# Optimization experiments

Measured on AMD Instinct MI355X. Metric: run time of the kernel, lower is better.

## Reference

```python
import jax, jax.numpy as jnp
import numpy as np

N = 200_000      # nodes
E = 6_400_000    # edges (avg degree 32)
G = 2_000        # graphs
SD = 10          # state_dim
ROUNDS = 3


def setup_inputs() -> dict:
    key = jax.random.key(0)
    ks = jax.random.split(key, 10)
    node_coordinates = jax.random.normal(ks[0], (N, 3), dtype=jnp.float32)
    node_graph_index = jnp.sort(jax.random.randint(ks[1], (N,), 0, G))
    node_from = jax.random.randint(ks[2], (E,), 0, N)
    node_to = jax.random.randint(ks[3], (E,), 0, N)
    edge_lengths = jax.random.uniform(ks[4], (E, 1), dtype=jnp.float32)
    edge_vectors = jax.random.normal(ks[5], (E, 3), dtype=jnp.float32)
    # message net: Linear(14 -> 10), torch default uniform init
    lim = 1.0 / np.sqrt(SD + 4)
    W_msg = jax.random.uniform(ks[6], (SD + 4, SD), minval=-lim, maxval=lim, dtype=jnp.float32)
    b_msg = jax.random.uniform(ks[7], (SD,), minval=-lim, maxval=lim, dtype=jnp.float32)
    # output net: Linear(10 -> 4), xavier_normal weight, default bias
    W_out = jax.random.normal(ks[8], (SD, 4), dtype=jnp.float32) * np.float32(np.sqrt(2.0 / (SD + 4)))
    lim_o = 1.0 / np.sqrt(SD)
    b_out = jax.random.uniform(ks[9], (4,), minval=-lim_o, maxval=lim_o, dtype=jnp.float32)
    return dict(node_coordinates=node_coordinates, edge_lengths=edge_lengths,
                edge_vectors=edge_vectors, W_msg=W_msg, b_msg=b_msg,
                W_out=W_out, b_out=b_out, node_from=node_from, node_to=node_to,
                node_graph_index=node_graph_index, num_nodes=N, num_graphs=G)


def reference(node_coordinates, edge_lengths, edge_vectors, W_msg, b_msg,
              W_out, b_out, node_from, node_to, node_graph_index,
              num_nodes, num_graphs):
    c_from = node_coordinates[node_from]                      # (E,3) gather
    c_to = node_coordinates[node_to]                          # (E,3) gather
    coord_sum = jnp.sum(jnp.abs(c_from), axis=1, keepdims=True)       # (E,1)
    dot1 = jnp.sum(c_from * c_to, axis=1, keepdims=True)              # (E,1)
    dot2 = jnp.sum(c_from * edge_vectors, axis=1, keepdims=True)      # (E,1)
    geo = jnp.concatenate([edge_lengths, coord_sum, dot1, dot2], axis=1)  # (E,4), identical every round

    state = jnp.zeros((num_nodes, SD), dtype=node_coordinates.dtype)
    for _ in range(ROUNDS):
        inp = jnp.concatenate([state[node_from], geo], axis=1)        # (E,14)
        msg = jnp.tanh(inp @ W_msg + b_msg)                           # (E,10)
        state = state + jax.ops.segment_sum(msg, node_to, num_segments=num_nodes)

    graph_state = jax.ops.segment_sum(state, node_graph_index, num_segments=num_graphs)  # (G,10)
    ev = graph_state @ W_out + b_out                                  # (G,4)
    gamma, v, alpha, beta = jnp.split(ev, 4, axis=1)
    sp = jax.nn.softplus
    return jnp.concatenate([gamma, sp(v), sp(alpha) + 1.0, sp(beta)], axis=1)
```

## Files before the change

kernel.cpp:

```cpp
#include <hip/hip_runtime.h>
#include <hip/hip_fp16.h>
#include <math.h>

#define SD 10
#define BSZ 64
#define EB 512
#define CTHR 1024
#define BINB 9
#define NBIN_MAX 512
#define HSZ 256
#define SCAP 10880

typedef unsigned uvec4 __attribute__((ext_vector_type(4)));
struct rec12 { unsigned x, y, z; };
union U32H2 { unsigned u; __half2 h; };

__device__ __forceinline__ float tanh_fast(float x) {
    float e = __expf(2.0f * x);
    float r = __builtin_amdgcn_rcpf(1.0f + e);
    return 1.0f - 2.0f * r;
}

__device__ __forceinline__ float softplus_f(float x) {
    return fmaxf(x, 0.0f) + log1pf(expf(-fabsf(x)));
}


__global__ __launch_bounds__(256) void coords4_kernel(
    const float* __restrict__ coords, float4* __restrict__ coords4, int N)
{
    int n = blockIdx.x * blockDim.x + threadIdx.x;
    if (n >= N) return;
    float4 c;
    c.x = coords[n * 3 + 0];
    c.y = coords[n * 3 + 1];
    c.z = coords[n * 3 + 2];
    c.w = fabsf(c.x) + fabsf(c.y) + fabsf(c.z);
    coords4[n] = c;
}


__global__ __launch_bounds__(CTHR) void pass1_kernel(
    const float* __restrict__ elen,
    const float* __restrict__ evec,
    const int* __restrict__ nfrom,
    const int* __restrict__ nto,
    unsigned* __restrict__ s1addr,
    rec12* __restrict__ payA,
    int E, int NBIN)
{
    __shared__ unsigned hbin[NBIN_MAX];
    __shared__ unsigned curbin[NBIN_MAX];
    int b = blockIdx.x, t = threadIdx.x;
    long long ebeg = (long long)E * b / EB;
    long long eend = (long long)E * (b + 1) / EB;

    if (t < NBIN_MAX) hbin[t] = 0;
    __syncthreads();
    for (long long e = ebeg + t; e < eend; e += CTHR)
        atomicAdd(&hbin[((unsigned)__builtin_nontemporal_load(&nto[e])) >> BINB], 1u);
    __syncthreads();
    {
        unsigned v = (t < NBIN_MAX) ? hbin[t] : 0u;
        for (int d = 1; d < NBIN_MAX; d <<= 1) {
            unsigned x = (t < NBIN_MAX && t >= d) ? hbin[t - d] : 0u;
            __syncthreads();
            if (t < NBIN_MAX) hbin[t] += x;
            __syncthreads();
        }
        if (t < NBIN_MAX) curbin[t] = (unsigned)ebeg + hbin[t] - v;
    }
    __syncthreads();
    if (t < NBIN) s1addr[(size_t)t * EB + b] = curbin[t];
    if (t == 0)  s1addr[(size_t)NBIN * EB + b] = (unsigned)eend;
    __syncthreads();

    for (long long e = ebeg + t; e < eend; e += CTHR) {
        int nf = __builtin_nontemporal_load(&nfrom[e]);
        int nt = __builtin_nontemporal_load(&nto[e]);
        float l  = __builtin_nontemporal_load(&elen[e]);
        float ex = __builtin_nontemporal_load(&evec[e * 3 + 0]);
        float ey = __builtin_nontemporal_load(&evec[e * 3 + 1]);
        float ez = __builtin_nontemporal_load(&evec[e * 3 + 2]);
        unsigned bin = ((unsigned)nt) >> BINB;
        unsigned pos = atomicAdd(&curbin[bin], 1u);
        U32H2 a, c;
        a.h = __floats2half2_rn(l, ex);
        c.h = __floats2half2_rn(ey, ez);
        rec12 r;
        r.x = (unsigned)nf | (((unsigned)nt & ((1u << BINB) - 1u)) << 18);
        r.y = a.u;
        r.z = c.u;
        payA[pos] = r;
    }
}

__global__ __launch_bounds__(256) void colsum_kernel(
    const unsigned* __restrict__ s1addr, unsigned* __restrict__ binsum)
{
    __shared__ unsigned red[256];
    int q = blockIdx.x, t = threadIdx.x;
    red[t] = s1addr[(size_t)q * EB + t] + s1addr[(size_t)q * EB + t + 256];
    __syncthreads();
    for (int d = 128; d > 0; d >>= 1) {
        if (t < d) red[t] += red[t + d];
        __syncthreads();
    }
    if (t == 0) binsum[q] = red[0];
}

__global__ __launch_bounds__(256) void binstart_kernel(
    const unsigned* __restrict__ binsum, unsigned* __restrict__ binstart,
    unsigned* __restrict__ nodestart, int NBIN, int E)
{
    int t = threadIdx.x;
    unsigned b0 = binsum[0];
    for (int q = t; q <= NBIN; q += 256) binstart[q] = binsum[q] - b0;
    if (t == 0) nodestart[(size_t)NBIN << BINB] = (unsigned)E;
}

__global__ __launch_bounds__(CTHR) void pass2_kernel(
    const unsigned* __restrict__ s1addr,
    const unsigned* __restrict__ binstart,
    const float4* __restrict__ coords4,
    const rec12* __restrict__ src,
    rec12* __restrict__ dst,
    unsigned* __restrict__ nodestart,
    int NBIN)
{
    __shared__ unsigned segst[EB];
    __shared__ unsigned spref[EB + 1];
    __shared__ unsigned hist[1 << BINB];
    __shared__ unsigned cur[1 << BINB];
    __shared__ rec12 stage[SCAP];
    int q = blockIdx.x, t = threadIdx.x;
    const unsigned KMASK = (1u << BINB) - 1u;

    if (t < EB) {
        unsigned st = s1addr[(size_t)q * EB + t];
        unsigned en = s1addr[(size_t)(q + 1) * EB + t];
        segst[t] = st;
        spref[t] = en - st;
    }
    if (t < (1 << BINB)) hist[t] = 0;
    __syncthreads();
    {
        unsigned v = (t < EB) ? spref[t] : 0u;
        for (int d = 1; d < EB; d <<= 1) {
            unsigned x = (t < EB && t >= d) ? spref[t - d] : 0u;
            __syncthreads();
            if (t < EB) spref[t] += x;
            __syncthreads();
        }
        unsigned incl = (t < EB) ? spref[t] : 0u;
        __syncthreads();
        if (t < EB) spref[t] = incl - v;
        if (t == EB - 1) spref[EB] = incl;
    }
    __syncthreads();
    unsigned len = spref[EB];
    unsigned obase = binstart[q];
    const unsigned* srcw = (const unsigned*)src;

    for (unsigned i = t; i < len; i += CTHR) {
        unsigned lo = 0, hi = EB;
#pragma unroll
        for (int s = 0; s < 9; s++) {
            unsigned mid = (lo + hi) >> 1;
            if (spref[mid] <= i) lo = mid; else hi = mid;
        }
        unsigned x0 = srcw[(size_t)(segst[lo] + (i - spref[lo])) * 3];
        atomicAdd(&hist[(x0 >> 18) & KMASK], 1u);
    }
    __syncthreads();
    unsigned hv = (t < (1 << BINB)) ? hist[t] : 0u;
    __syncthreads();
    for (int d = 1; d < (1 << BINB); d <<= 1) {
        unsigned x = (t < (1 << BINB) && t >= d) ? hist[t - d] : 0u;
        __syncthreads();
        if (t < (1 << BINB)) hist[t] += x;
        __syncthreads();
    }
    if (t < (1 << BINB)) {
        unsigned excl = hist[t] - hv;
        cur[t] = obase + excl;
        nodestart[((size_t)q << BINB) + t] = obase + excl;
    }
    __syncthreads();

    for (int h = 0; h < (1 << BINB) / HSZ; ++h) {
        unsigned kbeg = (unsigned)h * HSZ, kend = kbeg + HSZ;
        unsigned qs = kbeg ? hist[kbeg - 1] : 0u;
        unsigned qe = hist[kend - 1];
        unsigned qlen = qe - qs;
        unsigned qg = obase + qs;
        if (qlen <= (unsigned)SCAP) {
            for (unsigned i = t; i < len; i += CTHR) {
                unsigned lo = 0, hi = EB;
#pragma unroll
                for (int s = 0; s < 9; s++) {
                    unsigned mid = (lo + hi) >> 1;
                    if (spref[mid] <= i) lo = mid; else hi = mid;
                }
                rec12 p = src[segst[lo] + (i - spref[lo])];
                unsigned key = (p.x >> 18) & KMASK;
                if (key >= kbeg && key < kend) {
                    unsigned pos = atomicAdd(&cur[key], 1u);
                    stage[pos - qg] = p;
                }
            }
            __syncthreads();
            unsigned i = t;
            rec12 p0; float4 cf0;
            if (i < qlen) {
                p0 = stage[i];
                cf0 = coords4[p0.x & 0x3FFFFu];
            }
            while (i < qlen) {
                unsigned i1 = i + CTHR;
                rec12 p1 = p0; float4 cf1 = cf0;
                if (i1 < qlen) {
                    p1 = stage[i1];
                    cf1 = coords4[p1.x & 0x3FFFFu];
                }
                unsigned key = (p0.x >> 18) & KMASK;
                unsigned nf = p0.x & 0x3FFFFu;
                unsigned nt = ((unsigned)q << BINB) | key;
                float4 ct = coords4[nt];
                U32H2 ya, za;
                ya.u = p0.y; za.u = p0.z;
                float g0 = __low2float(ya.h), ev0 = __high2float(ya.h);
                float ev1 = __low2float(za.h), ev2 = __high2float(za.h);
                float g2 = cf0.x * ct.x + cf0.y * ct.y + cf0.z * ct.z;
                float g3 = cf0.x * ev0 + cf0.y * ev1 + cf0.z * ev2;
                U32H2 oy, oz;
                oy.h = __floats2half2_rn(g0, cf0.w);
                oz.h = __floats2half2_rn(g2, g3);
                rec12 r;
                r.x = nf | ((nt & (BSZ - 1u)) << 18);
                r.y = oy.u;
                r.z = oz.u;
                dst[qg + i] = r;
                i = i1; p0 = p1; cf0 = cf1;
            }
            __syncthreads();
        } else {
            for (unsigned i = t; i < len; i += CTHR) {
                unsigned lo = 0, hi = EB;
#pragma unroll
                for (int s = 0; s < 9; s++) {
                    unsigned mid = (lo + hi) >> 1;
                    if (spref[mid] <= i) lo = mid; else hi = mid;
                }
                rec12 p = src[segst[lo] + (i - spref[lo])];
                unsigned key = (p.x >> 18) & KMASK;
                if (key >= kbeg && key < kend) {
                    unsigned pos = atomicAdd(&cur[key], 1u);
                    unsigned nf = p.x & 0x3FFFFu;
                    unsigned nt = ((unsigned)q << BINB) | key;
                    float4 cf = coords4[nf];
                    float4 ct = coords4[nt];
                    U32H2 ya, za;
                    ya.u = p.y; za.u = p.z;
                    float g0 = __low2float(ya.h), ev0 = __high2float(ya.h);
                    float ev1 = __low2float(za.h), ev2 = __high2float(za.h);
                    float g2 = cf.x * ct.x + cf.y * ct.y + cf.z * ct.z;
                    float g3 = cf.x * ev0 + cf.y * ev1 + cf.z * ev2;
                    U32H2 oy, oz;
                    oy.h = __floats2half2_rn(g0, cf.w);
                    oz.h = __floats2half2_rn(g2, g3);
                    rec12 r;
                    r.x = nf | ((nt & (BSZ - 1u)) << 18);
                    r.y = oy.u;
                    r.z = oz.u;
                    dst[pos] = r;
                }
            }
            __syncthreads();
        }
    }
}


__global__ __launch_bounds__(256) void wstate_kernel(
    const float* __restrict__ state, const float* __restrict__ Wm,
    const float* __restrict__ bm, __half* __restrict__ wsth, int N)
{
    int n = blockIdx.x * blockDim.x + threadIdx.x;
    if (n >= N) return;
    const float2* sp = (const float2*)(state + (size_t)n * SD);
    float s[SD];
#pragma unroll
    for (int h = 0; h < 5; h++) { float2 v = sp[h]; s[2*h] = v.x; s[2*h+1] = v.y; }
    float t[SD];
#pragma unroll
    for (int j = 0; j < SD; j++) t[j] = bm[j];
#pragma unroll
    for (int k = 0; k < SD; k++) {
#pragma unroll
        for (int j = 0; j < SD; j++) t[j] += s[k] * Wm[k * SD + j];
    }
    unsigned* dp = (unsigned*)(wsth + (size_t)n * SD);
#pragma unroll
    for (int h = 0; h < 5; h++) {
        U32H2 cv;
        cv.h = __floats2half2_rn(t[2*h], t[2*h+1]);
        dp[h] = cv.u;
    }
}

template <bool FIRST>
__global__ __launch_bounds__(256) void round_run_kernel(
    const unsigned* __restrict__ nodestart,
    const rec12* __restrict__ payload,
    const float* __restrict__ Wm,
    const float* __restrict__ bm,
    const __half* __restrict__ wsth,
    const float* __restrict__ state_prev,
    float* __restrict__ state_next,
    int N, int E)
{
    __shared__ float acc[BSZ * SD];
    int k = blockIdx.x;
    for (int i = threadIdx.x; i < BSZ * SD; i += 256) acc[i] = 0.0f;

    int lane = threadIdx.x & 63;
    int wv = threadIdx.x >> 6;
    int grp0 = lane / 10;
    bool active = grp0 < 6;
    int grp = active ? grp0 : 5;
    int j = active ? (lane - grp0 * 10) : (lane - 60);

    float w0 = Wm[10 * SD + j];
    float w1 = Wm[11 * SD + j];
    float w2 = Wm[12 * SD + j];
    float w3 = Wm[13 * SD + j];
    float bb = bm[j];
    __syncthreads();

    unsigned beg = nodestart[(size_t)k << 6];
    unsigned end = nodestart[(size_t)(k + 1) << 6];
    unsigned len = end - beg;
    unsigned Q = (len + 3) >> 2;
    unsigned rbeg = beg + (unsigned)wv * Q;
    unsigned rend = rbeg + Q; if (rend > end) rend = end;
    unsigned eclamp = (unsigned)E - 1u;

    unsigned e0 = rbeg + (unsigned)grp;
    rec12 P0 = payload[e0 <= eclamp ? e0 : eclamp];
    unsigned e1 = e0 + 6;
    rec12 P1 = payload[e1 <= eclamp ? e1 : eclamp];
    float T0 = bb, T1 = bb;
    if (!FIRST) T0 = __half2float(wsth[(size_t)(P0.x & 0x3FFFFu) * SD + j]);

    int cur_lnt = -1;
    float accv = 0.0f;

    for (unsigned base = rbeg; base < rend; base += 6) {
        unsigned e2 = base + 12 + (unsigned)grp;
        rec12 P2 = payload[e2 <= eclamp ? e2 : eclamp];
        if (!FIRST) T1 = __half2float(wsth[(size_t)(P1.x & 0x3FFFFu) * SD + j]);
        unsigned e = base + (unsigned)grp;
        if (active && e < rend) {
            int lnt = (int)((P0.x >> 18) & (BSZ - 1));
            U32H2 c01, c23;
            c01.u = P0.y; c23.u = P0.z;
            float g0 = __low2float(c01.h), g1 = __high2float(c01.h);
            float g2 = __low2float(c23.h), g3 = __high2float(c23.h);
            float t = T0 + g0 * w0 + g1 * w1 + g2 * w2 + g3 * w3;
            if (lnt != cur_lnt) {
                if (cur_lnt >= 0) atomicAdd(&acc[cur_lnt * SD + j], accv);
                accv = 0.0f;
                cur_lnt = lnt;
            }
            accv += tanh_fast(t);
        }
        P0 = P1; P1 = P2; T0 = T1;
    }
    if (active && cur_lnt >= 0) atomicAdd(&acc[cur_lnt * SD + j], accv);
    __syncthreads();

    int base_o = k * BSZ * SD;
    int lim = N * SD - base_o;
    for (int i = threadIdx.x; i < BSZ * SD; i += 256) {
        if (i < lim) {
            float v = acc[i];
            if (!FIRST) v += state_prev[base_o + i];
            state_next[base_o + i] = v;
        }
    }
}


__global__ __launch_bounds__(256) void goff_kernel(
    const int* __restrict__ gidx, unsigned* __restrict__ goff, int N, int G)
{
    int n = blockIdx.x * blockDim.x + threadIdx.x;
    if (n >= N) return;
    int g = gidx[n];
    if (n == 0) {
        for (int q = 0; q <= g; q++) goff[q] = 0;
    } else {
        int gp = gidx[n - 1];
        for (int q = gp + 1; q <= g; q++) goff[q] = (unsigned)n;
    }
    if (n == N - 1) {
        for (int q = g + 1; q <= G; q++) goff[q] = (unsigned)N;
    }
}

__global__ __launch_bounds__(256) void gsum_kernel(
    const float* __restrict__ state, const unsigned* __restrict__ goff,
    float* __restrict__ gstate, int G)
{
    int tid = blockIdx.x * blockDim.x + threadIdx.x;
    if (tid >= G * SD * 4) return;
    int s = tid & 3;
    int rest = tid >> 2;
    int g = rest / SD;
    int j = rest - g * SD;
    unsigned beg = goff[g], end = goff[g + 1];
    unsigned len = end - beg;
    unsigned b0 = beg + (len * (unsigned)s) / 4u;
    unsigned b1 = beg + (len * (unsigned)(s + 1)) / 4u;
    float a = 0.0f;
    for (unsigned n = b0; n < b1; n++) a += state[(size_t)n * SD + j];
    atomicAdd(&gstate[(size_t)g * SD + j], a);
}

__global__ __launch_bounds__(256) void out_kernel(
    const float* __restrict__ gstate, const float* __restrict__ Wo,
    const float* __restrict__ bo, float* __restrict__ out, int G)
{
    int g = blockIdx.x * blockDim.x + threadIdx.x;
    if (g >= G) return;
    float s[SD];
#pragma unroll
    for (int k = 0; k < SD; k++) s[k] = gstate[(size_t)g * SD + k];
    float ev[4];
#pragma unroll
    for (int c = 0; c < 4; c++) {
        float a = bo[c];
#pragma unroll
        for (int k = 0; k < SD; k++) a += s[k] * Wo[k * 4 + c];
        ev[c] = a;
    }
    out[g * 4 + 0] = ev[0];
    out[g * 4 + 1] = softplus_f(ev[1]);
    out[g * 4 + 2] = softplus_f(ev[2]) + 1.0f;
    out[g * 4 + 3] = softplus_f(ev[3]);
}


template <bool FIRST>
__global__ __launch_bounds__(256) void edge_kernel_fb(
    const float* __restrict__ coords, const float* __restrict__ elen,
    const float* __restrict__ evec, const float* __restrict__ Wm,
    const float* __restrict__ bm, const int* __restrict__ nfrom,
    const int* __restrict__ nto, const float* __restrict__ state_prev,
    float* __restrict__ state_next, int E)
{
    int e = blockIdx.x * blockDim.x + threadIdx.x;
    if (e >= E) return;
    int nf = nfrom[e];
    int nt = nto[e];
    float cf0 = coords[nf*3+0], cf1 = coords[nf*3+1], cf2 = coords[nf*3+2];
    float ct0 = coords[nt*3+0], ct1 = coords[nt*3+1], ct2 = coords[nt*3+2];
    float ev0 = evec[e*3+0], ev1 = evec[e*3+1], ev2 = evec[e*3+2];
    float g0 = elen[e];
    float g1 = fabsf(cf0) + fabsf(cf1) + fabsf(cf2);
    float g2 = cf0*ct0 + cf1*ct1 + cf2*ct2;
    float g3 = cf0*ev0 + cf1*ev1 + cf2*ev2;
    float acc[SD];
#pragma unroll
    for (int j = 0; j < SD; j++) {
        acc[j] = bm[j] + g0*Wm[10*SD+j] + g1*Wm[11*SD+j] + g2*Wm[12*SD+j] + g3*Wm[13*SD+j];
    }
    if (!FIRST) {
        const float2* sp = (const float2*)(state_prev + (size_t)nf * SD);
        float s[SD];
#pragma unroll
        for (int h = 0; h < 5; h++) { float2 v = sp[h]; s[2*h] = v.x; s[2*h+1] = v.y; }
#pragma unroll
        for (int k = 0; k < SD; k++) {
#pragma unroll
            for (int j = 0; j < SD; j++) acc[j] += s[k] * Wm[k*SD+j];
        }
    }
    float* dst = state_next + (size_t)nt * SD;
#pragma unroll
    for (int j = 0; j < SD; j++) atomicAdd(dst + j, tanh_fast(acc[j]));
}

__global__ __launch_bounds__(256) void graph_reduce_fb(
    const float* __restrict__ state, const int* __restrict__ gidx,
    float* __restrict__ gstate, int N)
{
    int n = blockIdx.x * blockDim.x + threadIdx.x;
    if (n >= N) return;
    int g = gidx[n];
    const float2* sp = (const float2*)(state + (size_t)n * SD);
    float* dst = gstate + (size_t)g * SD;
#pragma unroll
    for (int h = 0; h < 5; h++) {
        float2 v = sp[h];
        atomicAdd(dst + 2*h, v.x);
        atomicAdd(dst + 2*h + 1, v.y);
    }
}


extern "C" void kernel_launch(void* const* d_in, const int* in_sizes, int n_in,
                              void* d_out, int out_size, void* d_ws, size_t ws_size,
                              hipStream_t stream) {
    const float* coords = (const float*)d_in[0];
    const float* elen   = (const float*)d_in[1];
    const float* evec   = (const float*)d_in[2];
    const float* Wm     = (const float*)d_in[3];
    const float* bm     = (const float*)d_in[4];
    const float* Wo     = (const float*)d_in[5];
    const float* bo     = (const float*)d_in[6];
    const int* nfrom    = (const int*)d_in[7];
    const int* nto      = (const int*)d_in[8];
    const int* gidx     = (const int*)d_in[9];

    const int E = in_sizes[1];
    const int N = in_sizes[9];
    const int G = out_size / 4;

    const int NBIN = (N + (1 << BINB) - 1) >> BINB;
    const int NB   = (N + BSZ - 1) / BSZ;

    const int BLK = 256;
    const int ng = (N + BLK - 1) / BLK;
    const int gg = (G + BLK - 1) / BLK;

    auto align256 = [](size_t x) { return (x + 255) & ~(size_t)255; };
    const size_t state_bytes = align256((size_t)N * SD * sizeof(float));
    const size_t wst_bytes   = align256((size_t)N * SD * sizeof(__half) + 256);
    const size_t payA_bytes  = align256((size_t)E * sizeof(rec12) + 256);
    const size_t payB_bytes  = align256((size_t)E * sizeof(rec12) + 256);
    const size_t s1a_bytes   = align256((size_t)(NBIN_MAX + 1) * EB * sizeof(unsigned));
    const size_t bsum_bytes  = align256((size_t)(NBIN_MAX + 1) * sizeof(unsigned));
    const size_t nst_bytes   = align256(((size_t)NBIN_MAX * (1 << BINB) + 2) * sizeof(unsigned));
    const size_t goff_bytes  = align256((size_t)(G + 1) * sizeof(unsigned));
    const size_t gst_bytes   = align256((size_t)G * SD * sizeof(float));
    const size_t c4_bytes    = align256((size_t)N * sizeof(float4));

    size_t o = 0;
    char* w = (char*)d_ws;
    float* stateA      = (float*)(w + o);    o += state_bytes;
    float* stateB      = (float*)(w + o);    o += state_bytes;
    __half* wsth       = (__half*)(w + o);   o += wst_bytes;
    rec12* payA        = (rec12*)(w + o);    o += payA_bytes;
    rec12* payB        = (rec12*)(w + o);    o += payB_bytes;
    unsigned* s1addr   = (unsigned*)(w + o); o += s1a_bytes;
    unsigned* binsum   = (unsigned*)(w + o); o += bsum_bytes;
    unsigned* binstart = (unsigned*)(w + o); o += bsum_bytes;
    unsigned* nodestart= (unsigned*)(w + o); o += nst_bytes;
    unsigned* goff     = (unsigned*)(w + o); o += goff_bytes;
    float* gstate      = (float*)(w + o);    o += gst_bytes;
    float4* coords4    = (float4*)(w + o);   o += c4_bytes;

    if (o <= ws_size && NBIN <= NBIN_MAX && N < (1 << 18)) {
        coords4_kernel<<<ng, BLK, 0, stream>>>(coords, coords4, N);
        pass1_kernel<<<EB, CTHR, 0, stream>>>(elen, evec, nfrom, nto,
                                              s1addr, payA, E, NBIN);
        colsum_kernel<<<NBIN + 1, 256, 0, stream>>>(s1addr, binsum);
        binstart_kernel<<<1, 256, 0, stream>>>(binsum, binstart, nodestart, NBIN, E);
        pass2_kernel<<<NBIN, CTHR, 0, stream>>>(s1addr, binstart, coords4,
                                                payA, payB, nodestart, NBIN);
        round_run_kernel<true><<<NB, BLK, 0, stream>>>(nodestart, payB, Wm, bm,
                                                       wsth, stateB, stateA, N, E);
        wstate_kernel<<<ng, BLK, 0, stream>>>(stateA, Wm, bm, wsth, N);
        round_run_kernel<false><<<NB, BLK, 0, stream>>>(nodestart, payB, Wm, bm,
                                                        wsth, stateA, stateB, N, E);
        wstate_kernel<<<ng, BLK, 0, stream>>>(stateB, Wm, bm, wsth, N);
        round_run_kernel<false><<<NB, BLK, 0, stream>>>(nodestart, payB, Wm, bm,
                                                        wsth, stateB, stateA, N, E);
        hipMemsetAsync(gstate, 0, (size_t)G * SD * sizeof(float), stream);
        goff_kernel<<<ng, BLK, 0, stream>>>(gidx, goff, N, G);
        gsum_kernel<<<(G * SD * 4 + BLK - 1) / BLK, BLK, 0, stream>>>(stateA, goff, gstate, G);
        out_kernel<<<gg, BLK, 0, stream>>>(gstate, Wo, bo, (float*)d_out, G);
    } else {
        const int eg = (E + BLK - 1) / BLK;
        float* gstateF = (float*)(w + 2 * state_bytes);
        hipMemsetAsync(stateA, 0, state_bytes, stream);
        hipMemsetAsync(gstateF, 0, (size_t)G * SD * sizeof(float), stream);
        edge_kernel_fb<true><<<eg, BLK, 0, stream>>>(coords, elen, evec, Wm, bm,
                                                     nfrom, nto, stateA, stateA, E);
        hipMemcpyAsync(stateB, stateA, state_bytes, hipMemcpyDeviceToDevice, stream);
        edge_kernel_fb<false><<<eg, BLK, 0, stream>>>(coords, elen, evec, Wm, bm,
                                                      nfrom, nto, stateA, stateB, E);
        hipMemcpyAsync(stateA, stateB, state_bytes, hipMemcpyDeviceToDevice, stream);
        edge_kernel_fb<false><<<eg, BLK, 0, stream>>>(coords, elen, evec, Wm, bm,
                                                      nfrom, nto, stateB, stateA, E);
        graph_reduce_fb<<<ng, BLK, 0, stream>>>(stateA, gidx, gstateF, N);
        out_kernel<<<gg, BLK, 0, stream>>>(gstateF, Wo, bo, (float*)d_out, G);
    }
}
```

Measured before the change: 680.0 us.

## Shrink sort bins to 256 nodes and scatter each bin in a single pass

```diff
diff --git a/kernel.cpp b/kernel.cpp
--- a/kernel.cpp
+++ b/kernel.cpp
@@ -4,11 +4,10 @@
 
 #define SD 10
 #define BSZ 64
-#define EB 512
+#define EB 256
 #define CTHR 1024
-#define BINB 9
-#define NBIN_MAX 512
-#define HSZ 256
+#define BINB 8
+#define NBIN_MAX 1024
 #define SCAP 10880
 
 typedef unsigned uvec4 __attribute__((ext_vector_type(4)));
@@ -55,20 +54,20 @@
     long long ebeg = (long long)E * b / EB;
     long long eend = (long long)E * (b + 1) / EB;
 
-    if (t < NBIN_MAX) hbin[t] = 0;
+    hbin[t] = 0;
     __syncthreads();
     for (long long e = ebeg + t; e < eend; e += CTHR)
         atomicAdd(&hbin[((unsigned)__builtin_nontemporal_load(&nto[e])) >> BINB], 1u);
     __syncthreads();
     {
-        unsigned v = (t < NBIN_MAX) ? hbin[t] : 0u;
+        unsigned v = hbin[t];
         for (int d = 1; d < NBIN_MAX; d <<= 1) {
-            unsigned x = (t < NBIN_MAX && t >= d) ? hbin[t - d] : 0u;
+            unsigned x = (t >= d) ? hbin[t - d] : 0u;
             __syncthreads();
-            if (t < NBIN_MAX) hbin[t] += x;
+            hbin[t] += x;
             __syncthreads();
         }
-        if (t < NBIN_MAX) curbin[t] = (unsigned)ebeg + hbin[t] - v;
+        curbin[t] = (unsigned)ebeg + hbin[t] - v;
     }
     __syncthreads();
     if (t < NBIN) s1addr[(size_t)t * EB + b] = curbin[t];
@@ -100,7 +99,7 @@
 {
     __shared__ unsigned red[256];
     int q = blockIdx.x, t = threadIdx.x;
-    red[t] = s1addr[(size_t)q * EB + t] + s1addr[(size_t)q * EB + t + 256];
+    red[t] = s1addr[(size_t)q * EB + t];
     __syncthreads();
     for (int d = 128; d > 0; d >>= 1) {
         if (t < d) red[t] += red[t + d];
@@ -165,7 +164,7 @@
     for (unsigned i = t; i < len; i += CTHR) {
         unsigned lo = 0, hi = EB;
 #pragma unroll
-        for (int s = 0; s < 9; s++) {
+        for (int s = 0; s < 8; s++) {
             unsigned mid = (lo + hi) >> 1;
             if (spref[mid] <= i) lo = mid; else hi = mid;
         }
@@ -173,110 +172,97 @@
         atomicAdd(&hist[(x0 >> 18) & KMASK], 1u);
     }
     __syncthreads();
-    unsigned hv = (t < (1 << BINB)) ? hist[t] : 0u;
-    __syncthreads();
-    for (int d = 1; d < (1 << BINB); d <<= 1) {
-        unsigned x = (t < (1 << BINB) && t >= d) ? hist[t - d] : 0u;
+    {
+        unsigned hv = (t < (1 << BINB)) ? hist[t] : 0u;
+        for (int d = 1; d < (1 << BINB); d <<= 1) {
+            unsigned x = (t < (1 << BINB) && t >= d) ? hist[t - d] : 0u;
+            __syncthreads();
+            if (t < (1 << BINB)) hist[t] += x;
+            __syncthreads();
+        }
+        if (t < (1 << BINB)) {
+            unsigned excl = hist[t] - hv;
+            cur[t] = obase + excl;
+            nodestart[((size_t)q << BINB) + t] = obase + excl;
+        }
+    }
+    __syncthreads();
+
+    if (len <= (unsigned)SCAP) {
+        for (unsigned i = t; i < len; i += CTHR) {
+            unsigned lo = 0, hi = EB;
+#pragma unroll
+            for (int s = 0; s < 8; s++) {
+                unsigned mid = (lo + hi) >> 1;
+                if (spref[mid] <= i) lo = mid; else hi = mid;
+            }
+            rec12 p = src[segst[lo] + (i - spref[lo])];
+            unsigned pos = atomicAdd(&cur[(p.x >> 18) & KMASK], 1u);
+            stage[pos - obase] = p;
+        }
         __syncthreads();
-        if (t < (1 << BINB)) hist[t] += x;
-        __syncthreads();
-    }
-    if (t < (1 << BINB)) {
-        unsigned excl = hist[t] - hv;
-        cur[t] = obase + excl;
-        nodestart[((size_t)q << BINB) + t] = obase + excl;
-    }
-    __syncthreads();
-
-    for (int h = 0; h < (1 << BINB) / HSZ; ++h) {
-        unsigned kbeg = (unsigned)h * HSZ, kend = kbeg + HSZ;
-        unsigned qs = kbeg ? hist[kbeg - 1] : 0u;
-        unsigned qe = hist[kend - 1];
-        unsigned qlen = qe - qs;
-        unsigned qg = obase + qs;
-        if (qlen <= (unsigned)SCAP) {
-            for (unsigned i = t; i < len; i += CTHR) {
-                unsigned lo = 0, hi = EB;
-#pragma unroll
-                for (int s = 0; s < 9; s++) {
-                    unsigned mid = (lo + hi) >> 1;
-                    if (spref[mid] <= i) lo = mid; else hi = mid;
-                }
-                rec12 p = src[segst[lo] + (i - spref[lo])];
-                unsigned key = (p.x >> 18) & KMASK;
-                if (key >= kbeg && key < kend) {
-                    unsigned pos = atomicAdd(&cur[key], 1u);
-                    stage[pos - qg] = p;
-                }
+        unsigned i = t;
+        rec12 p0; float4 cf0;
+        if (i < len) {
+            p0 = stage[i];
+            cf0 = coords4[p0.x & 0x3FFFFu];
+        }
+        while (i < len) {
+            unsigned i1 = i + CTHR;
+            rec12 p1 = p0; float4 cf1 = cf0;
+            if (i1 < len) {
+                p1 = stage[i1];
+                cf1 = coords4[p1.x & 0x3FFFFu];
             }
-            __syncthreads();
-            unsigned i = t;
-            rec12 p0; float4 cf0;
-            if (i < qlen) {
-                p0 = stage[i];
-                cf0 = coords4[p0.x & 0x3FFFFu];
+            unsigned key = (p0.x >> 18) & KMASK;
+            unsigned nf = p0.x & 0x3FFFFu;
+            unsigned nt = ((unsigned)q << BINB) | key;
+            float4 ct = coords4[nt];
+            U32H2 ya, za;
+            ya.u = p0.y; za.u = p0.z;
+            float g0 = __low2float(ya.h), ev0 = __high2float(ya.h);
+            float ev1 = __low2float(za.h), ev2 = __high2float(za.h);
+            float g2 = cf0.x * ct.x + cf0.y * ct.y + cf0.z * ct.z;
+            float g3 = cf0.x * ev0 + cf0.y * ev1 + cf0.z * ev2;
+            U32H2 oy, oz;
+            oy.h = __floats2half2_rn(g0, cf0.w);
+            oz.h = __floats2half2_rn(g2, g3);
+            rec12 r;
+            r.x = nf | ((nt & (BSZ - 1u)) << 18);
+            r.y = oy.u;
+            r.z = oz.u;
+            dst[obase + i] = r;
+            i = i1; p0 = p1; cf0 = cf1;
+        }
+    } else {
+        for (unsigned i = t; i < len; i += CTHR) {
+            unsigned lo = 0, hi = EB;
+#pragma unroll
+            for (int s = 0; s < 8; s++) {
+                unsigned mid = (lo + hi) >> 1;
+                if (spref[mid] <= i) lo = mid; else hi = mid;
             }
-            while (i < qlen) {
-                unsigned i1 = i + CTHR;
-                rec12 p1 = p0; float4 cf1 = cf0;
-                if (i1 < qlen) {
-                    p1 = stage[i1];
-                    cf1 = coords4[p1.x & 0x3FFFFu];
-                }
-                unsigned key = (p0.x >> 18) & KMASK;
-                unsigned nf = p0.x & 0x3FFFFu;
-                unsigned nt = ((unsigned)q << BINB) | key;
-                float4 ct = coords4[nt];
-                U32H2 ya, za;
-                ya.u = p0.y; za.u = p0.z;
-                float g0 = __low2float(ya.h), ev0 = __high2float(ya.h);
-                float ev1 = __low2float(za.h), ev2 = __high2float(za.h);
-                float g2 = cf0.x * ct.x + cf0.y * ct.y + cf0.z * ct.z;
-                float g3 = cf0.x * ev0 + cf0.y * ev1 + cf0.z * ev2;
-                U32H2 oy, oz;
-                oy.h = __floats2half2_rn(g0, cf0.w);
-                oz.h = __floats2half2_rn(g2, g3);
-                rec12 r;
-                r.x = nf | ((nt & (BSZ - 1u)) << 18);
-                r.y = oy.u;
-                r.z = oz.u;
-                dst[qg + i] = r;
-                i = i1; p0 = p1; cf0 = cf1;
-            }
-            __syncthreads();
-        } else {
-            for (unsigned i = t; i < len; i += CTHR) {
-                unsigned lo = 0, hi = EB;
-#pragma unroll
-                for (int s = 0; s < 9; s++) {
-                    unsigned mid = (lo + hi) >> 1;
-                    if (spref[mid] <= i) lo = mid; else hi = mid;
-                }
-                rec12 p = src[segst[lo] + (i - spref[lo])];
-                unsigned key = (p.x >> 18) & KMASK;
-                if (key >= kbeg && key < kend) {
-                    unsigned pos = atomicAdd(&cur[key], 1u);
-                    unsigned nf = p.x & 0x3FFFFu;
-                    unsigned nt = ((unsigned)q << BINB) | key;
-                    float4 cf = coords4[nf];
-                    float4 ct = coords4[nt];
-                    U32H2 ya, za;
-                    ya.u = p.y; za.u = p.z;
-                    float g0 = __low2float(ya.h), ev0 = __high2float(ya.h);
-                    float ev1 = __low2float(za.h), ev2 = __high2float(za.h);
-                    float g2 = cf.x * ct.x + cf.y * ct.y + cf.z * ct.z;
-                    float g3 = cf.x * ev0 + cf.y * ev1 + cf.z * ev2;
-                    U32H2 oy, oz;
-                    oy.h = __floats2half2_rn(g0, cf.w);
-                    oz.h = __floats2half2_rn(g2, g3);
-                    rec12 r;
-                    r.x = nf | ((nt & (BSZ - 1u)) << 18);
-                    r.y = oy.u;
-                    r.z = oz.u;
-                    dst[pos] = r;
-                }
-            }
-            __syncthreads();
+            rec12 p = src[segst[lo] + (i - spref[lo])];
+            unsigned key = (p.x >> 18) & KMASK;
+            unsigned pos = atomicAdd(&cur[key], 1u);
+            unsigned nf = p.x & 0x3FFFFu;
+            unsigned nt = ((unsigned)q << BINB) | key;
+            float4 cf = coords4[nf];
+            float4 ct = coords4[nt];
+            U32H2 ya, za;
+            ya.u = p.y; za.u = p.z;
+            float g0 = __low2float(ya.h), ev0 = __high2float(ya.h);
+            float ev1 = __low2float(za.h), ev2 = __high2float(za.h);
+            float g2 = cf.x * ct.x + cf.y * ct.y + cf.z * ct.z;
+            float g3 = cf.x * ev0 + cf.y * ev1 + cf.z * ev2;
+            U32H2 oy, oz;
+            oy.h = __floats2half2_rn(g0, cf.w);
+            oz.h = __floats2half2_rn(g2, g3);
+            rec12 r;
+            r.x = nf | ((nt & (BSZ - 1u)) << 18);
+            r.y = oy.u;
+            r.z = oz.u;
+            dst[pos] = r;
         }
     }
 }
```

Measured after the change: 670.1 us. About the same (-1.4%).
